# Performance work log

Measured on AMD Instinct MI355X. Metric: run time of the kernel, lower is better.

## Reference

```python
import jax, jax.numpy as jnp
import numpy as np

B, L, H, N, CH = 8, 2048, 512, 64, 1


def setup_inputs() -> dict:
    key = jax.random.key(0)
    ks = jax.random.split(key, 7)
    # S4D-Lin style init: w = -0.5 + i*pi*n, with slight noise on the real part
    w_re = -(0.5 + 0.1 * jax.random.uniform(ks[0], (H, N), dtype=jnp.float32))
    w_im = jnp.broadcast_to(jnp.pi * jnp.arange(N, dtype=jnp.float32), (H, N)).copy()
    C_re = jax.random.normal(ks[1], (CH, H, N), dtype=jnp.float32)
    C_im = jax.random.normal(ks[2], (CH, H, N), dtype=jnp.float32)
    D = jax.random.normal(ks[3], (CH, H), dtype=jnp.float32)
    # log-uniform dt in [1e-3, 1e-1]
    log_dt = jax.random.uniform(ks[4], (H,), dtype=jnp.float32,
                                minval=jnp.log(1e-3), maxval=jnp.log(1e-1))
    dt = jnp.exp(log_dt)
    u = jax.random.normal(ks[5], (B, L, H), dtype=jnp.float32)
    return {"u": u, "w_re": w_re, "w_im": w_im, "C_re": C_re,
            "C_im": C_im, "D": D, "dt": dt}


def reference(u, w_re, w_im, C_re, C_im, D, dt):
    # u: [B, L, H] -> [B, H, L]
    uT = jnp.swapaxes(u, -1, -2)
    l = uT.shape[-1]
    h = dt.shape[-1]
    w = (w_re + 1j * w_im).astype(jnp.complex64)          # [t, n]
    v = h // w.shape[0]
    w = jnp.tile(w, (v, 1))                                # [h, n]
    C = (C_re + 1j * C_im).astype(jnp.complex64)           # [c, h, n]
    # --- kernel generation ---
    dtA = w * dt[:, None]                                  # [h, n]
    K = jnp.arange(l) * dtA[..., None]                     # [h, n, l]
    Cs = C * ((jnp.exp(dtA) - 1.0) / w)                    # [c, h, n]
    k = 2.0 * jnp.einsum('chn,hnl->chl', Cs, jnp.exp(K)).real  # [c, h, l]
    # --- FFT convolution ---
    k_f = jnp.fft.rfft(k, n=2 * l - 1)                     # [c, h, l]
    u_f = jnp.fft.rfft(uT, n=2 * l - 1)                    # [B, h, l]
    y_f = jnp.einsum('...hl,chl->...chl', u_f, k_f)        # [B, c, h, l]
    y = jnp.fft.irfft(y_f, n=2 * l)[..., :l]               # [B, c, h, l]
    # skip connection
    y = y + jnp.einsum('...hl,ch->...chl', uT, D)
    # '... c h l -> ... l c h'
    return jnp.moveaxis(y, (-3, -2, -1), (-2, -1, -3))
```

## Files before the change

### kernel.cpp

```cpp
#include <hip/hip_runtime.h>
#include <hip/hip_bf16.h>
#include <math.h>


namespace {
constexpr int cB = 8;
constexpr int cL = 2048;
constexpr int cH = 512;
constexpr int cN = 64;
constexpr int M1 = 4095;
constexpr int M2 = 4096;
constexpr int BH = cB * cH;
constexpr int MA = BH + cH;

constexpr size_t S0   = 2 * ((size_t)cH * cN * 6);
constexpr size_t S_B1 = S0;
constexpr size_t S_A  = S_B1 + (size_t)4096 * 2048;
constexpr size_t S_T2 = S_A  + (size_t)MA * 2048;
constexpr size_t S_U  = S_T2 + (size_t)2048 * 4096;
}

typedef __attribute__((ext_vector_type(8))) short short8;
typedef __attribute__((ext_vector_type(4))) short sh4;
typedef __attribute__((ext_vector_type(4))) float f32x4;

static __device__ inline short f2bf(float x) {
    __hip_bfloat16 h = __float2bfloat16(x);
    return *reinterpret_cast<short*>(&h);
}
static __device__ inline float bf2f(short s) {
    return __uint_as_float(((unsigned int)(unsigned short)s) << 16);
}
static __device__ __forceinline__ void load_lds16(const short* g, short* l) {
    __builtin_amdgcn_global_load_lds(
        (const __attribute__((address_space(1))) void*)g,
        (__attribute__((address_space(3))) void*)l, 16, 0, 0);
}
#define WAIT_LGKM0() do { asm volatile("s_waitcnt lgkmcnt(0)" ::: "memory"); \
                          __builtin_amdgcn_sched_barrier(0); } while (0)
#define WAIT_VM(n)   do { asm volatile("s_waitcnt vmcnt(" #n ")" ::: "memory"); \
                          __builtin_amdgcn_sched_barrier(0); } while (0)

__global__ __launch_bounds__(256) void k_tabs(short* __restrict__ Wb)
{
    if (blockIdx.x < 2048) {
        int j  = blockIdx.x;
        int t0 = threadIdx.x * 8;
        int p  = (int)(((long)j * t0) % M1);
        short8 vc, vs;
#pragma unroll
        for (int i = 0; i < 8; ++i) {
            float s, c;
            sincosf((6.283185307179586f / (float)M1) * (float)p, &s, &c);
            vc[i] = f2bf(c); vs[i] = f2bf(s);
            p += j; if (p >= M1) p -= M1;
        }
        *(short8*)&Wb[S_B1 + (size_t)(2 * j)     * 2048 + t0] = vc;
        *(short8*)&Wb[S_B1 + (size_t)(2 * j + 1) * 2048 + t0] = vs;
    } else {
        int t  = blockIdx.x - 2048;
        int j0 = threadIdx.x * 8;
        int p  = (t * j0) & (M2 - 1);
        short8 vc, vs;
#pragma unroll
        for (int i = 0; i < 8; ++i) {
            float s, c;
            sincosf((6.283185307179586f / (float)M2) * (float)p, &s, &c);
            vc[i] = f2bf(c); vs[i] = f2bf(s);
            p = (p + t) & (M2 - 1);
        }
        *(short8*)&Wb[S_T2 + (size_t)t * 4096 + j0]        = vc;
        *(short8*)&Wb[S_T2 + (size_t)t * 4096 + 2048 + j0] = vs;
    }
}

__global__ __launch_bounds__(256) void k_trans(const float* __restrict__ u,
                                               short* __restrict__ Wb)
{
    __shared__ float tile[64][65];
    int t0 = blockIdx.x * 64;
    int h0 = blockIdx.y * 64;
    int b  = blockIdx.z;
    int cx = threadIdx.x & 63, r0 = threadIdx.x >> 6;
#pragma unroll
    for (int i = 0; i < 16; ++i) {
        int row = r0 + i * 4;
        tile[row][cx] = u[((size_t)b * cL + t0 + row) * cH + h0 + cx];
    }
    __syncthreads();
    short* A = Wb + S_A;
#pragma unroll
    for (int i = 0; i < 16; ++i) {
        int hrow = r0 + i * 4;
        A[(size_t)(b * cH + h0 + hrow) * 2048 + t0 + cx] = f2bf(tile[cx][hrow]);
    }
}

__global__ __launch_bounds__(256) void k_kgen(
    const float* __restrict__ w_re, const float* __restrict__ w_im,
    const float* __restrict__ C_re, const float* __restrict__ C_im,
    const float* __restrict__ dt, short* __restrict__ Wb)
{
    __shared__ float md[cN * 6];
    int h = blockIdx.x, tid = threadIdx.x;
    if (tid < cN) {
        int idx = h * cN + tid;
        double dtv = dt[h];
        double wr = w_re[idx], wi = w_im[idx];
        double ar = wr * dtv, ai = wi * dtv;
        double er = exp(ar);
        double zs, zc; sincos(ai, &zs, &zc);
        double zr = er * zc, zi = er * zs;
        double nr = zr - 1.0, ni = zi;
        double inv = 1.0 / (wr * wr + wi * wi);
        double gr = (nr * wr + ni * wi) * inv;
        double gi = (ni * wr - nr * wi) * inv;
        double cr = C_re[idx], ci = C_im[idx];
        md[tid*6+0] = (float)(cr * gr - ci * gi);
        md[tid*6+1] = (float)(cr * gi + ci * gr);
        md[tid*6+2] = (float)zr; md[tid*6+3] = (float)zi;
        md[tid*6+4] = (float)ar; md[tid*6+5] = (float)ai;
    }
    __syncthreads();
    int t0 = tid * 8;
    float acc[8] = {0.f, 0.f, 0.f, 0.f, 0.f, 0.f, 0.f, 0.f};
    for (int n = 0; n < cN; ++n) {
        float csr = md[n*6+0], csi = md[n*6+1];
        float zr  = md[n*6+2], zi  = md[n*6+3];
        float ar  = md[n*6+4], ai  = md[n*6+5];
        float mag = expf(ar * (float)t0);
        double ph = fmod((double)ai * (double)t0, 6.283185307179586);
        float s, c; sincosf((float)ph, &s, &c);
        float pr = mag * c, pi = mag * s;
#pragma unroll
        for (int i = 0; i < 8; ++i) {
            acc[i] += csr * pr - csi * pi;
            float tr = pr * zr - pi * zi;
            pi = pr * zi + pi * zr;
            pr = tr;
        }
    }
    short8 v;
#pragma unroll
    for (int i = 0; i < 8; ++i) v[i] = f2bf(2.f * acc[i]);
    *reinterpret_cast<short8*>(&Wb[S_A + (size_t)(BH + h) * 2048 + t0]) = v;
}

__device__ __forceinline__ void gemm8p_core(
    const short* __restrict__ Ag, int lda,
    const short* __restrict__ Bg, int ldb,
    int m0, int n0, int nt, short* lds, f32x4 (&acc)[4][4][2])
{
    const int tid  = threadIdx.x;
    const int wave = tid >> 6, lane = tid & 63;
    const int wm = wave >> 2, wn = wave & 3;
    const int lm = lane & 15, lk = lane >> 4;
    const int srow8 = lane >> 3;
    const int scol  = (lane & 7) * 8;

    auto stage = [&](const short* G, int ldg, int row0, int half, int kt, int sb) {
        short* l0 = lds + sb + (size_t)((kt & 1) * 2 + half) * 8192;
#pragma unroll
        for (int q = 0; q < 2; ++q) {
            int chunk = wave * 2 + q;
            int r = chunk * 8 + srow8;
            int c = scol ^ ((r & 7) << 3);
            load_lds16(G + (size_t)(row0 + half * 128 + r) * ldg + kt * 64 + c,
                       l0 + chunk * 512);
        }
    };
    auto rdA = [&](int qa, int kt, int mi, int kk) -> short8 {
        int rl = wm * 64 + mi * 16 + lm;
        int c  = (kk * 32 + lk * 8) ^ ((rl & 7) << 3);
        return *(const short8*)(lds + (size_t)((kt & 1) * 2 + qa) * 8192 + rl * 64 + c);
    };
    auto rdB = [&](int qb, int kt, int ni, int kk) -> short8 {
        int rl = wn * 32 + ni * 16 + lm;
        int c  = (kk * 32 + lk * 8) ^ ((rl & 7) << 3);
        return *(const short8*)(lds + 32768 + (size_t)((kt & 1) * 2 + qb) * 8192 + rl * 64 + c);
    };

    stage(Ag, lda, m0, 0, 0, 0);
    stage(Bg, ldb, n0, 0, 0, 32768);
    stage(Bg, ldb, n0, 1, 0, 32768);
    stage(Ag, lda, m0, 1, 0, 0);
    if (nt > 1) { stage(Ag, lda, m0, 0, 1, 0); stage(Bg, ldb, n0, 1, 1, 32768); }
    WAIT_VM(4);
    __builtin_amdgcn_s_barrier();

    short8 a[4][2], b[2][2];
    for (int t = 0; t < nt; ++t) {
#pragma unroll
        for (int mi = 0; mi < 4; ++mi) { a[mi][0] = rdA(0, t, mi, 0); a[mi][1] = rdA(0, t, mi, 1); }
#pragma unroll
        for (int ni = 0; ni < 2; ++ni) { b[ni][0] = rdB(0, t, ni, 0); b[ni][1] = rdB(0, t, ni, 1); }
        if (t + 1 < nt) stage(Ag, lda, m0, 1, t + 1, 0);
        __builtin_amdgcn_s_barrier();
        WAIT_LGKM0();
        __builtin_amdgcn_s_setprio(1);
#pragma unroll
        for (int kk = 0; kk < 2; ++kk)
#pragma unroll
        for (int ni = 0; ni < 2; ++ni)
#pragma unroll
        for (int mi = 0; mi < 4; ++mi)
            acc[0][mi][ni] = __builtin_amdgcn_mfma_f32_16x16x32_bf16(a[mi][kk], b[ni][kk], acc[0][mi][ni], 0, 0, 0);
        __builtin_amdgcn_s_setprio(0);
        __builtin_amdgcn_s_barrier();
#pragma unroll
        for (int ni = 0; ni < 2; ++ni) { b[ni][0] = rdB(1, t, ni, 0); b[ni][1] = rdB(1, t, ni, 1); }
        if (t + 1 < nt) stage(Bg, ldb, n0, 0, t + 1, 32768);
        __builtin_amdgcn_s_barrier();
        WAIT_LGKM0();
        __builtin_amdgcn_s_setprio(1);
#pragma unroll
        for (int kk = 0; kk < 2; ++kk)
#pragma unroll
        for (int ni = 0; ni < 2; ++ni)
#pragma unroll
        for (int mi = 0; mi < 4; ++mi)
            acc[1][mi][ni] = __builtin_amdgcn_mfma_f32_16x16x32_bf16(a[mi][kk], b[ni][kk], acc[1][mi][ni], 0, 0, 0);
        __builtin_amdgcn_s_setprio(0);
        __builtin_amdgcn_s_barrier();
#pragma unroll
        for (int mi = 0; mi < 4; ++mi) { a[mi][0] = rdA(1, t, mi, 0); a[mi][1] = rdA(1, t, mi, 1); }
        if (t + 2 < nt) stage(Ag, lda, m0, 0, t + 2, 0);
        __builtin_amdgcn_s_barrier();
        WAIT_LGKM0();
        __builtin_amdgcn_s_setprio(1);
#pragma unroll
        for (int kk = 0; kk < 2; ++kk)
#pragma unroll
        for (int ni = 0; ni < 2; ++ni)
#pragma unroll
        for (int mi = 0; mi < 4; ++mi)
            acc[3][mi][ni] = __builtin_amdgcn_mfma_f32_16x16x32_bf16(a[mi][kk], b[ni][kk], acc[3][mi][ni], 0, 0, 0);
        __builtin_amdgcn_s_setprio(0);
        __builtin_amdgcn_s_barrier();
#pragma unroll
        for (int ni = 0; ni < 2; ++ni) { b[ni][0] = rdB(0, t, ni, 0); b[ni][1] = rdB(0, t, ni, 1); }
        if (t + 2 < nt) stage(Bg, ldb, n0, 1, t + 2, 32768);
        if (t < nt - 2) { WAIT_VM(4); } else { WAIT_VM(0); }
        __builtin_amdgcn_s_barrier();
        WAIT_LGKM0();
        __builtin_amdgcn_s_setprio(1);
#pragma unroll
        for (int kk = 0; kk < 2; ++kk)
#pragma unroll
        for (int ni = 0; ni < 2; ++ni)
#pragma unroll
        for (int mi = 0; mi < 4; ++mi)
            acc[2][mi][ni] = __builtin_amdgcn_mfma_f32_16x16x32_bf16(a[mi][kk], b[ni][kk], acc[2][mi][ni], 0, 0, 0);
        __builtin_amdgcn_s_setprio(0);
        __builtin_amdgcn_s_barrier();
    }
}

__global__ __launch_bounds__(512, 2) void k_fwd8(short* __restrict__ Wb)
{
    __shared__ short lds_s[65536];
    int tile = (blockIdx.x & 7) * 32 + (blockIdx.x >> 3);
    const int m0 = (tile >> 4) * 256, n0 = (tile & 15) * 256;
    const int tid = threadIdx.x;
    const int wave = tid >> 6, lane = tid & 63;
    const int wm = wave >> 2, wn = wave & 3;
    const int lm = lane & 15, lk = lane >> 4;

    f32x4 acc[4][4][2] = {};
    gemm8p_core(Wb + S_A, 2048, Wb + S_B1, 2048, m0, n0, 32, lds_s, acc);

    short* Ys = Wb + S_U;
    const short* KF = Wb + S_U;
    short (*M)[136] = (short(*)[136])lds_s;
    for (int q = 0; q < 4; ++q) {
        __syncthreads();
#pragma unroll
        for (int mi = 0; mi < 4; ++mi)
#pragma unroll
        for (int ni = 0; ni < 2; ++ni)
#pragma unroll
        for (int r = 0; r < 4; ++r)
            M[wm * 64 + mi * 16 + lk * 4 + r][wn * 32 + ni * 16 + lm] =
                f2bf(acc[q][mi][ni][r]);
        __syncthreads();
        const int jwin = (n0 >> 1) + (q & 1) * 64;
#pragma unroll
        for (int pass = 0; pass < 4; ++pass) {
            int rl = pass * 32 + (tid >> 4);
            int p0 = (tid & 15) * 4;
            int rowg = m0 + (q >> 1) * 128 + rl;
            int h = rowg & (cH - 1);
            short8 kf8 = *(const short8*)&KF[(size_t)(4096 + h) * 4096 + 2 * (jwin + p0)];
            short8 m8  = *(const short8*)&M[rl][2 * p0];
            sh4 yr4, yi4;
#pragma unroll
            for (int i = 0; i < 4; ++i) {
                float C  = bf2f(m8[2*i]),  S  = bf2f(m8[2*i+1]);
                float Ck = bf2f(kf8[2*i]), Sk = bf2f(kf8[2*i+1]);
                int j = jwin + p0 + i;
                float sc = (j == 0 ? 1.0f : 2.0f) * (1.0f / (float)M2);
                yr4[i] = f2bf(sc * (Ck * C - Sk * S));
                yi4[i] = f2bf(sc * (Ck * S + Sk * C));
            }
            *(sh4*)&Ys[(size_t)rowg * 4096 + jwin + p0]        = yr4;
            *(sh4*)&Ys[(size_t)rowg * 4096 + 2048 + jwin + p0] = yi4;
        }
    }
}

__global__ __launch_bounds__(256, 2) void k_kfg(short* __restrict__ Wb)
{
    __shared__ __align__(16) short As[128][32];
    __shared__ __align__(16) short Bs[128][32];
    const short* A = Wb + S_A;
    const short* B = Wb + S_B1;
    short* U = Wb + S_U;
    const int tid = threadIdx.x;
    const int m0 = 4096 + blockIdx.y * 128, n0 = blockIdx.x * 128;
    const int wave = tid >> 6, lane = tid & 63;
    const int wr = wave >> 1, wc = wave & 1;
    const int lm = lane & 15, lk = lane >> 4;
    const int srow = lane >> 2, scol = (lane & 3) * 8;

    f32x4 acc[4][4] = {};
    for (int k0 = 0; k0 < 2048; k0 += 32) {
        __syncthreads();
        {
            int c0 = wave * 2;
            load_lds16(&A[(size_t)(m0 + c0*16      + srow)*2048 + k0 + scol], &As[c0*16][0]);
            load_lds16(&A[(size_t)(m0 + c0*16 + 16 + srow)*2048 + k0 + scol], &As[c0*16+16][0]);
            load_lds16(&B[(size_t)(n0 + c0*16      + srow)*2048 + k0 + scol], &Bs[c0*16][0]);
            load_lds16(&B[(size_t)(n0 + c0*16 + 16 + srow)*2048 + k0 + scol], &Bs[c0*16+16][0]);
        }
        __syncthreads();
        short8 a[4];
#pragma unroll
        for (int mi = 0; mi < 4; ++mi)
            a[mi] = *(const short8*)&As[wr*64 + mi*16 + lm][lk*8];
#pragma unroll
        for (int ni = 0; ni < 4; ++ni) {
            short8 b = *(const short8*)&Bs[wc*64 + ni*16 + lm][lk*8];
#pragma unroll
            for (int mi = 0; mi < 4; ++mi)
                acc[mi][ni] = __builtin_amdgcn_mfma_f32_16x16x32_bf16(a[mi], b, acc[mi][ni], 0, 0, 0);
        }
    }
#pragma unroll
    for (int mi = 0; mi < 4; ++mi)
#pragma unroll
    for (int ni = 0; ni < 4; ++ni)
#pragma unroll
    for (int r = 0; r < 4; ++r) {
        int row = m0 + wr*64 + mi*16 + lk*4 + r;
        int col = n0 + wc*64 + ni*16 + lm;
        U[(size_t)row * 4096 + col] = f2bf(acc[mi][ni][r]);
    }
}

__global__ __launch_bounds__(512, 1) void k_invB(const float* __restrict__ u,
                                                 const float* __restrict__ Dp,
                                                 short* __restrict__ Wb,
                                                 float* __restrict__ out)
{
    __shared__ short lds_s[49152];
    int tile = (blockIdx.x & 7) * 32 + (blockIdx.x >> 3);
    const int m0 = (tile >> 4) * 256;
    const int n0 = (tile & 15) * 128;
    const int tid = threadIdx.x;
    const int wave = tid >> 6, lane = tid & 63;
    const int wm = wave >> 2, wn = wave & 3;
    const int lm = lane & 15, lk = lane >> 4;
    const int srow8 = lane >> 3;
    const int scol  = (lane & 7) * 8;
    constexpr int nt = 64;
    short* lds = lds_s;
    const short* Ag = Wb + S_U;
    const short* Bg = Wb + S_T2;

    auto stageA = [&](int half, int kt) {
        short* l0 = lds + (size_t)((kt & 1) * 2 + half) * 8192;
#pragma unroll
        for (int q = 0; q < 2; ++q) {
            int chunk = wave * 2 + q;
            int r = chunk * 8 + srow8;
            int c = scol ^ ((r & 7) << 3);
            load_lds16(Ag + (size_t)(m0 + half * 128 + r) * 4096 + kt * 64 + c,
                       l0 + chunk * 512);
        }
    };
    auto stageB = [&](int kt) {
        short* l0 = lds + 32768 + (size_t)(kt & 1) * 8192;
#pragma unroll
        for (int q = 0; q < 2; ++q) {
            int chunk = wave * 2 + q;
            int r = chunk * 8 + srow8;
            int c = scol ^ ((r & 7) << 3);
            load_lds16(Bg + (size_t)(n0 + r) * 4096 + kt * 64 + c,
                       l0 + chunk * 512);
        }
    };
    auto rdA = [&](int half, int kt, int mi, int kk) -> short8 {
        int rl = wm * 64 + mi * 16 + lm;
        int c  = (kk * 32 + lk * 8) ^ ((rl & 7) << 3);
        return *(const short8*)(lds + (size_t)((kt & 1) * 2 + half) * 8192 + rl * 64 + c);
    };
    auto rdB = [&](int kt, int ni, int kk) -> short8 {
        int rl = wn * 32 + ni * 16 + lm;
        int c  = (kk * 32 + lk * 8) ^ ((rl & 7) << 3);
        return *(const short8*)(lds + 32768 + (size_t)(kt & 1) * 8192 + rl * 64 + c);
    };

    f32x4 acc[2][4][2] = {};

    stageA(0, 0);
    stageB(0);
    stageA(1, 0);
    WAIT_VM(2);
    __builtin_amdgcn_s_barrier();

    short8 a[4][2], b[2][2];
    for (int t = 0; t < nt; ++t) {
#pragma unroll
        for (int mi = 0; mi < 4; ++mi) { a[mi][0] = rdA(0, t, mi, 0); a[mi][1] = rdA(0, t, mi, 1); }
#pragma unroll
        for (int ni = 0; ni < 2; ++ni) { b[ni][0] = rdB(t, ni, 0); b[ni][1] = rdB(t, ni, 1); }
        if (t + 1 < nt) stageB(t + 1);
        __builtin_amdgcn_s_barrier();
        WAIT_LGKM0();
        __builtin_amdgcn_s_setprio(1);
#pragma unroll
        for (int kk = 0; kk < 2; ++kk)
#pragma unroll
        for (int ni = 0; ni < 2; ++ni)
#pragma unroll
        for (int mi = 0; mi < 4; ++mi)
            acc[0][mi][ni] = __builtin_amdgcn_mfma_f32_16x16x32_bf16(a[mi][kk], b[ni][kk], acc[0][mi][ni], 0, 0, 0);
        __builtin_amdgcn_s_setprio(0);
        if (t + 1 < nt) { WAIT_VM(2); } else { WAIT_VM(0); }
        __builtin_amdgcn_s_barrier();
#pragma unroll
        for (int mi = 0; mi < 4; ++mi) { a[mi][0] = rdA(1, t, mi, 0); a[mi][1] = rdA(1, t, mi, 1); }
        if (t + 1 < nt) { stageA(0, t + 1); stageA(1, t + 1); }
        __builtin_amdgcn_s_barrier();
        WAIT_LGKM0();
        __builtin_amdgcn_s_setprio(1);
#pragma unroll
        for (int kk = 0; kk < 2; ++kk)
#pragma unroll
        for (int ni = 0; ni < 2; ++ni)
#pragma unroll
        for (int mi = 0; mi < 4; ++mi)
            acc[1][mi][ni] = __builtin_amdgcn_mfma_f32_16x16x32_bf16(a[mi][kk], b[ni][kk], acc[1][mi][ni], 0, 0, 0);
        __builtin_amdgcn_s_setprio(0);
        WAIT_VM(2);
        __builtin_amdgcn_s_barrier();
    }

    const int b_  = m0 >> 9;
    const int h00 = m0 & 511;
    float (*T)[132] = (float(*)[132])lds_s;
#pragma unroll
    for (int q = 0; q < 2; ++q) {
        __syncthreads();
#pragma unroll
        for (int mi = 0; mi < 4; ++mi)
#pragma unroll
        for (int ni = 0; ni < 2; ++ni) {
            int tl = wn * 32 + ni * 16 + lm;
            int hl = wm * 64 + mi * 16 + lk * 4;
            *(float4*)&T[tl][hl] = *(float4*)&acc[q][mi][ni];
        }
        __syncthreads();
        int hg = h00 + q * 128 + (tid & 31) * 4;
        float4 dv = *(const float4*)&Dp[hg];
#pragma unroll
        for (int it = 0; it < 8; ++it) {
            int tl = (tid >> 5) + it * 16;
            int tg = n0 + tl;
            size_t gidx = ((size_t)b_ * cL + tg) * cH + hg;
            float4 uv = *(const float4*)&u[gidx];
            float4 yv = *(float4*)&T[tl][(tid & 31) * 4];
            yv.x += dv.x * uv.x;
            yv.y += dv.y * uv.y;
            yv.z += dv.z * uv.z;
            yv.w += dv.w * uv.w;
            *(float4*)&out[gidx] = yv;
        }
    }
}

extern "C" void kernel_launch(void* const* d_in, const int* in_sizes, int n_in,
                              void* d_out, int out_size, void* d_ws, size_t ws_size,
                              hipStream_t stream) {
    const float* u    = (const float*)d_in[0];
    const float* w_re = (const float*)d_in[1];
    const float* w_im = (const float*)d_in[2];
    const float* C_re = (const float*)d_in[3];
    const float* C_im = (const float*)d_in[4];
    const float* Dp   = (const float*)d_in[5];
    const float* dt   = (const float*)d_in[6];
    float* out = (float*)d_out;
    short* Wb  = (short*)d_ws;

    hipLaunchKernelGGL(k_tabs,  dim3(4096), dim3(256), 0, stream, Wb);
    hipLaunchKernelGGL(k_trans, dim3(cL / 64, cH / 64, cB), dim3(256), 0, stream, u, Wb);
    hipLaunchKernelGGL(k_kgen,  dim3(cH), dim3(256), 0, stream,
                       w_re, w_im, C_re, C_im, dt, Wb);
    hipLaunchKernelGGL(k_kfg,   dim3(32, 4), dim3(256), 0, stream, Wb);
    hipLaunchKernelGGL(k_fwd8,  dim3(256), dim3(512), 0, stream, Wb);
    hipLaunchKernelGGL(k_invB,  dim3(256), dim3(512), 0, stream, u, Dp, Wb, out);
}
```

Baseline: 228.4 us.

## Merge prep kernels and deepen GEMM prefetch pipelines with extra stage buffers

Merges the twiddle-table, transpose and kernel-generation launches into one k_prep kernel that dispatches on block index, removing two launches and their serialization. The gemm8p_core loop now prefetches two k-tiles ahead with separate A/B register sets, which reorders the quadrant MFMAs to reuse fragments. k_invB gets a third B stage buffer (LDS grows to 57344 shorts) so B can be prefetched three tiles ahead. In exchange, larger LDS and register use may lower occupancy, and the vmcnt wait counts must match the new issue order exactly.

```diff
diff --git a/kernel.cpp b/kernel.cpp
--- a/kernel.cpp
+++ b/kernel.cpp
@@ -40,12 +40,19 @@
                           __builtin_amdgcn_sched_barrier(0); } while (0)
 #define WAIT_VM(n)   do { asm volatile("s_waitcnt vmcnt(" #n ")" ::: "memory"); \
                           __builtin_amdgcn_sched_barrier(0); } while (0)
-
-__global__ __launch_bounds__(256) void k_tabs(short* __restrict__ Wb)
+#define BAR() __builtin_amdgcn_s_barrier()
+
+__global__ __launch_bounds__(256) void k_prep(
+    const float* __restrict__ u,
+    const float* __restrict__ w_re, const float* __restrict__ w_im,
+    const float* __restrict__ C_re, const float* __restrict__ C_im,
+    const float* __restrict__ dt, short* __restrict__ Wb)
 {
-    if (blockIdx.x < 2048) {
-        int j  = blockIdx.x;
-        int t0 = threadIdx.x * 8;
+    __shared__ char smc[64 * 65 * 4];
+    int bid = blockIdx.x, tid = threadIdx.x;
+    if (bid < 2048) {
+        int j  = bid;
+        int t0 = tid * 8;
         int p  = (int)(((long)j * t0) % M1);
         short8 vc, vs;
 #pragma unroll
@@ -57,9 +64,9 @@
         }
         *(short8*)&Wb[S_B1 + (size_t)(2 * j)     * 2048 + t0] = vc;
         *(short8*)&Wb[S_B1 + (size_t)(2 * j + 1) * 2048 + t0] = vs;
-    } else {
-        int t  = blockIdx.x - 2048;
-        int j0 = threadIdx.x * 8;
+    } else if (bid < 4096) {
+        int t  = bid - 2048;
+        int j0 = tid * 8;
         int p  = (t * j0) & (M2 - 1);
         short8 vc, vs;
 #pragma unroll
@@ -71,80 +78,77 @@
         }
         *(short8*)&Wb[S_T2 + (size_t)t * 4096 + j0]        = vc;
         *(short8*)&Wb[S_T2 + (size_t)t * 4096 + 2048 + j0] = vs;
-    }
-}
-
-__global__ __launch_bounds__(256) void k_trans(const float* __restrict__ u,
-                                               short* __restrict__ Wb)
-{
-    __shared__ float tile[64][65];
-    int t0 = blockIdx.x * 64;
-    int h0 = blockIdx.y * 64;
-    int b  = blockIdx.z;
-    int cx = threadIdx.x & 63, r0 = threadIdx.x >> 6;
-#pragma unroll
-    for (int i = 0; i < 16; ++i) {
-        int row = r0 + i * 4;
-        tile[row][cx] = u[((size_t)b * cL + t0 + row) * cH + h0 + cx];
-    }
-    __syncthreads();
-    short* A = Wb + S_A;
-#pragma unroll
-    for (int i = 0; i < 16; ++i) {
-        int hrow = r0 + i * 4;
-        A[(size_t)(b * cH + h0 + hrow) * 2048 + t0 + cx] = f2bf(tile[cx][hrow]);
-    }
-}
-
-__global__ __launch_bounds__(256) void k_kgen(
-    const float* __restrict__ w_re, const float* __restrict__ w_im,
-    const float* __restrict__ C_re, const float* __restrict__ C_im,
-    const float* __restrict__ dt, short* __restrict__ Wb)
-{
-    __shared__ float md[cN * 6];
-    int h = blockIdx.x, tid = threadIdx.x;
-    if (tid < cN) {
-        int idx = h * cN + tid;
-        double dtv = dt[h];
-        double wr = w_re[idx], wi = w_im[idx];
-        double ar = wr * dtv, ai = wi * dtv;
-        double er = exp(ar);
-        double zs, zc; sincos(ai, &zs, &zc);
-        double zr = er * zc, zi = er * zs;
-        double nr = zr - 1.0, ni = zi;
-        double inv = 1.0 / (wr * wr + wi * wi);
-        double gr = (nr * wr + ni * wi) * inv;
-        double gi = (ni * wr - nr * wi) * inv;
-        double cr = C_re[idx], ci = C_im[idx];
-        md[tid*6+0] = (float)(cr * gr - ci * gi);
-        md[tid*6+1] = (float)(cr * gi + ci * gr);
-        md[tid*6+2] = (float)zr; md[tid*6+3] = (float)zi;
-        md[tid*6+4] = (float)ar; md[tid*6+5] = (float)ai;
-    }
-    __syncthreads();
-    int t0 = tid * 8;
-    float acc[8] = {0.f, 0.f, 0.f, 0.f, 0.f, 0.f, 0.f, 0.f};
-    for (int n = 0; n < cN; ++n) {
-        float csr = md[n*6+0], csi = md[n*6+1];
-        float zr  = md[n*6+2], zi  = md[n*6+3];
-        float ar  = md[n*6+4], ai  = md[n*6+5];
-        float mag = expf(ar * (float)t0);
-        double ph = fmod((double)ai * (double)t0, 6.283185307179586);
-        float s, c; sincosf((float)ph, &s, &c);
-        float pr = mag * c, pi = mag * s;
-#pragma unroll
-        for (int i = 0; i < 8; ++i) {
-            acc[i] += csr * pr - csi * pi;
-            float tr = pr * zr - pi * zi;
-            pi = pr * zi + pi * zr;
-            pr = tr;
-        }
-    }
-    short8 v;
-#pragma unroll
-    for (int i = 0; i < 8; ++i) v[i] = f2bf(2.f * acc[i]);
-    *reinterpret_cast<short8*>(&Wb[S_A + (size_t)(BH + h) * 2048 + t0]) = v;
-}
+    } else if (bid < 6144) {
+        float (*tile)[65] = (float(*)[65])smc;
+        int bid2 = bid - 4096;
+        int t0 = (bid2 & 31) * 64;
+        int h0 = ((bid2 >> 5) & 7) * 64;
+        int b  = bid2 >> 8;
+        int cx = tid & 63, r0 = tid >> 6;
+#pragma unroll
+        for (int i = 0; i < 16; ++i) {
+            int row = r0 + i * 4;
+            tile[row][cx] = u[((size_t)b * cL + t0 + row) * cH + h0 + cx];
+        }
+        __syncthreads();
+        short* A = Wb + S_A;
+#pragma unroll
+        for (int i = 0; i < 16; ++i) {
+            int hrow = r0 + i * 4;
+            A[(size_t)(b * cH + h0 + hrow) * 2048 + t0 + cx] = f2bf(tile[cx][hrow]);
+        }
+    } else {
+        float* md = (float*)smc;
+        int h = bid - 6144;
+        if (tid < cN) {
+            int idx = h * cN + tid;
+            double dtv = dt[h];
+            double wr = w_re[idx], wi = w_im[idx];
+            double ar = wr * dtv, ai = wi * dtv;
+            double er = exp(ar);
+            double zs, zc; sincos(ai, &zs, &zc);
+            double zr = er * zc, zi = er * zs;
+            double nr = zr - 1.0, ni = zi;
+            double inv = 1.0 / (wr * wr + wi * wi);
+            double gr = (nr * wr + ni * wi) * inv;
+            double gi = (ni * wr - nr * wi) * inv;
+            double cr = C_re[idx], ci = C_im[idx];
+            md[tid*6+0] = (float)(cr * gr - ci * gi);
+            md[tid*6+1] = (float)(cr * gi + ci * gr);
+            md[tid*6+2] = (float)zr; md[tid*6+3] = (float)zi;
+            md[tid*6+4] = (float)ar; md[tid*6+5] = (float)ai;
+        }
+        __syncthreads();
+        int t0 = tid * 8;
+        float acc[8] = {0.f, 0.f, 0.f, 0.f, 0.f, 0.f, 0.f, 0.f};
+        for (int n = 0; n < cN; ++n) {
+            float csr = md[n*6+0], csi = md[n*6+1];
+            float zr  = md[n*6+2], zi  = md[n*6+3];
+            float ar  = md[n*6+4], ai  = md[n*6+5];
+            float mag = expf(ar * (float)t0);
+            double ph = fmod((double)ai * (double)t0, 6.283185307179586);
+            float s, c; sincosf((float)ph, &s, &c);
+            float pr = mag * c, pi = mag * s;
+#pragma unroll
+            for (int i = 0; i < 8; ++i) {
+                acc[i] += csr * pr - csi * pi;
+                float tr = pr * zr - pi * zi;
+                pi = pr * zi + pi * zr;
+                pr = tr;
+            }
+        }
+        short8 v;
+#pragma unroll
+        for (int i = 0; i < 8; ++i) v[i] = f2bf(2.f * acc[i]);
+        *reinterpret_cast<short8*>(&Wb[S_A + (size_t)(BH + h) * 2048 + t0]) = v;
+    }
+}
+
+#define MFMA16(AR, BR, ACC) \
+    _Pragma("unroll") for (int kk = 0; kk < 2; ++kk) \
+    _Pragma("unroll") for (int ni = 0; ni < 2; ++ni) \
+    _Pragma("unroll") for (int mi = 0; mi < 4; ++mi) \
+        ACC[mi][ni] = __builtin_amdgcn_mfma_f32_16x16x32_bf16(AR[mi][kk], BR[ni][kk], ACC[mi][ni], 0, 0, 0);
 
 __device__ __forceinline__ void gemm8p_core(
     const short* __restrict__ Ag, int lda,
@@ -184,75 +188,52 @@
     stage(Bg, ldb, n0, 0, 0, 32768);
     stage(Bg, ldb, n0, 1, 0, 32768);
     stage(Ag, lda, m0, 1, 0, 0);
-    if (nt > 1) { stage(Ag, lda, m0, 0, 1, 0); stage(Bg, ldb, n0, 1, 1, 32768); }
-    WAIT_VM(4);
-    __builtin_amdgcn_s_barrier();
-
-    short8 a[4][2], b[2][2];
+    stage(Ag, lda, m0, 0, 1, 0);
+    stage(Bg, ldb, n0, 0, 1, 32768);
+    stage(Bg, ldb, n0, 1, 1, 32768);
+    stage(Ag, lda, m0, 1, 1, 0);
+    WAIT_VM(12);
+    BAR();
+
+    short8 a0[4][2], a1[4][2], b0[2][2], b1[2][2];
     for (int t = 0; t < nt; ++t) {
-#pragma unroll
-        for (int mi = 0; mi < 4; ++mi) { a[mi][0] = rdA(0, t, mi, 0); a[mi][1] = rdA(0, t, mi, 1); }
-#pragma unroll
-        for (int ni = 0; ni < 2; ++ni) { b[ni][0] = rdB(0, t, ni, 0); b[ni][1] = rdB(0, t, ni, 1); }
-        if (t + 1 < nt) stage(Ag, lda, m0, 1, t + 1, 0);
-        __builtin_amdgcn_s_barrier();
+        const bool st = (t + 2 < nt);
+#pragma unroll
+        for (int mi = 0; mi < 4; ++mi) { a0[mi][0] = rdA(0, t, mi, 0); a0[mi][1] = rdA(0, t, mi, 1); }
+#pragma unroll
+        for (int ni = 0; ni < 2; ++ni) { b0[ni][0] = rdB(0, t, ni, 0); b0[ni][1] = rdB(0, t, ni, 1); }
+        BAR();
         WAIT_LGKM0();
         __builtin_amdgcn_s_setprio(1);
-#pragma unroll
-        for (int kk = 0; kk < 2; ++kk)
-#pragma unroll
-        for (int ni = 0; ni < 2; ++ni)
-#pragma unroll
-        for (int mi = 0; mi < 4; ++mi)
-            acc[0][mi][ni] = __builtin_amdgcn_mfma_f32_16x16x32_bf16(a[mi][kk], b[ni][kk], acc[0][mi][ni], 0, 0, 0);
-        __builtin_amdgcn_s_setprio(0);
-        __builtin_amdgcn_s_barrier();
-#pragma unroll
-        for (int ni = 0; ni < 2; ++ni) { b[ni][0] = rdB(1, t, ni, 0); b[ni][1] = rdB(1, t, ni, 1); }
-        if (t + 1 < nt) stage(Bg, ldb, n0, 0, t + 1, 32768);
-        __builtin_amdgcn_s_barrier();
+        MFMA16(a0, b0, acc[0]);
+        __builtin_amdgcn_s_setprio(0);
+        if (st) { WAIT_VM(10); } else { WAIT_VM(0); }
+        BAR();
+#pragma unroll
+        for (int ni = 0; ni < 2; ++ni) { b1[ni][0] = rdB(1, t, ni, 0); b1[ni][1] = rdB(1, t, ni, 1); }
+        if (st) { stage(Ag, lda, m0, 0, t + 2, 0); stage(Bg, ldb, n0, 0, t + 2, 32768); }
+        BAR();
         WAIT_LGKM0();
         __builtin_amdgcn_s_setprio(1);
-#pragma unroll
-        for (int kk = 0; kk < 2; ++kk)
-#pragma unroll
-        for (int ni = 0; ni < 2; ++ni)
-#pragma unroll
-        for (int mi = 0; mi < 4; ++mi)
-            acc[1][mi][ni] = __builtin_amdgcn_mfma_f32_16x16x32_bf16(a[mi][kk], b[ni][kk], acc[1][mi][ni], 0, 0, 0);
-        __builtin_amdgcn_s_setprio(0);
-        __builtin_amdgcn_s_barrier();
-#pragma unroll
-        for (int mi = 0; mi < 4; ++mi) { a[mi][0] = rdA(1, t, mi, 0); a[mi][1] = rdA(1, t, mi, 1); }
-        if (t + 2 < nt) stage(Ag, lda, m0, 0, t + 2, 0);
-        __builtin_amdgcn_s_barrier();
+        MFMA16(a0, b1, acc[1]);
+        __builtin_amdgcn_s_setprio(0);
+        if (st) { WAIT_VM(12); } else { WAIT_VM(0); }
+        BAR();
+#pragma unroll
+        for (int mi = 0; mi < 4; ++mi) { a1[mi][0] = rdA(1, t, mi, 0); a1[mi][1] = rdA(1, t, mi, 1); }
+        if (st) stage(Bg, ldb, n0, 1, t + 2, 32768);
+        BAR();
         WAIT_LGKM0();
         __builtin_amdgcn_s_setprio(1);
-#pragma unroll
-        for (int kk = 0; kk < 2; ++kk)
-#pragma unroll
-        for (int ni = 0; ni < 2; ++ni)
-#pragma unroll
-        for (int mi = 0; mi < 4; ++mi)
-            acc[3][mi][ni] = __builtin_amdgcn_mfma_f32_16x16x32_bf16(a[mi][kk], b[ni][kk], acc[3][mi][ni], 0, 0, 0);
-        __builtin_amdgcn_s_setprio(0);
-        __builtin_amdgcn_s_barrier();
-#pragma unroll
-        for (int ni = 0; ni < 2; ++ni) { b[ni][0] = rdB(0, t, ni, 0); b[ni][1] = rdB(0, t, ni, 1); }
-        if (t + 2 < nt) stage(Bg, ldb, n0, 1, t + 2, 32768);
-        if (t < nt - 2) { WAIT_VM(4); } else { WAIT_VM(0); }
-        __builtin_amdgcn_s_barrier();
-        WAIT_LGKM0();
-        __builtin_amdgcn_s_setprio(1);
-#pragma unroll
-        for (int kk = 0; kk < 2; ++kk)
-#pragma unroll
-        for (int ni = 0; ni < 2; ++ni)
-#pragma unroll
-        for (int mi = 0; mi < 4; ++mi)
-            acc[2][mi][ni] = __builtin_amdgcn_mfma_f32_16x16x32_bf16(a[mi][kk], b[ni][kk], acc[2][mi][ni], 0, 0, 0);
-        __builtin_amdgcn_s_setprio(0);
-        __builtin_amdgcn_s_barrier();
+        MFMA16(a1, b1, acc[3]);
+        __builtin_amdgcn_s_setprio(0);
+        BAR();
+        if (st) stage(Ag, lda, m0, 1, t + 2, 0);
+        __builtin_amdgcn_s_setprio(1);
+        MFMA16(a1, b0, acc[2]);
+        __builtin_amdgcn_s_setprio(0);
+        if (st) { WAIT_VM(12); } else { WAIT_VM(0); }
+        BAR();
     }
 }
 
@@ -362,7 +343,7 @@
                                                  short* __restrict__ Wb,
                                                  float* __restrict__ out)
 {
-    __shared__ short lds_s[49152];
+    __shared__ short lds_s[57344];
     int tile = (blockIdx.x & 7) * 32 + (blockIdx.x >> 3);
     const int m0 = (tile >> 4) * 256;
     const int n0 = (tile & 15) * 128;
@@ -388,8 +369,8 @@
                        l0 + chunk * 512);
         }
     };
-    auto stageB = [&](int kt) {
-        short* l0 = lds + 32768 + (size_t)(kt & 1) * 8192;
+    auto stageB = [&](int kt, int slot) {
+        short* l0 = lds + 32768 + (size_t)slot * 8192;
 #pragma unroll
         for (int q = 0; q < 2; ++q) {
             int chunk = wave * 2 + q;
@@ -404,56 +385,51 @@
         int c  = (kk * 32 + lk * 8) ^ ((rl & 7) << 3);
         return *(const short8*)(lds + (size_t)((kt & 1) * 2 + half) * 8192 + rl * 64 + c);
     };
-    auto rdB = [&](int kt, int ni, int kk) -> short8 {
+    auto rdB = [&](int slot, int ni, int kk) -> short8 {
         int rl = wn * 32 + ni * 16 + lm;
         int c  = (kk * 32 + lk * 8) ^ ((rl & 7) << 3);
-        return *(const short8*)(lds + 32768 + (size_t)(kt & 1) * 8192 + rl * 64 + c);
+        return *(const short8*)(lds + 32768 + (size_t)slot * 8192 + rl * 64 + c);
     };
 
     f32x4 acc[2][4][2] = {};
 
     stageA(0, 0);
-    stageB(0);
+    stageB(0, 0);
     stageA(1, 0);
-    WAIT_VM(2);
-    __builtin_amdgcn_s_barrier();
+    stageA(0, 1);
+    stageB(1, 1);
+    stageB(2, 2);
+    WAIT_VM(6);
+    BAR();
 
     short8 a[4][2], b[2][2];
+    int bs = 0;
     for (int t = 0; t < nt; ++t) {
+        const bool deep = (t + 3 < nt);
 #pragma unroll
         for (int mi = 0; mi < 4; ++mi) { a[mi][0] = rdA(0, t, mi, 0); a[mi][1] = rdA(0, t, mi, 1); }
 #pragma unroll
-        for (int ni = 0; ni < 2; ++ni) { b[ni][0] = rdB(t, ni, 0); b[ni][1] = rdB(t, ni, 1); }
-        if (t + 1 < nt) stageB(t + 1);
-        __builtin_amdgcn_s_barrier();
+        for (int ni = 0; ni < 2; ++ni) { b[ni][0] = rdB(bs, ni, 0); b[ni][1] = rdB(bs, ni, 1); }
+        if (t + 1 < nt) stageA(1, t + 1);
+        BAR();
         WAIT_LGKM0();
         __builtin_amdgcn_s_setprio(1);
-#pragma unroll
-        for (int kk = 0; kk < 2; ++kk)
-#pragma unroll
-        for (int ni = 0; ni < 2; ++ni)
-#pragma unroll
-        for (int mi = 0; mi < 4; ++mi)
-            acc[0][mi][ni] = __builtin_amdgcn_mfma_f32_16x16x32_bf16(a[mi][kk], b[ni][kk], acc[0][mi][ni], 0, 0, 0);
-        __builtin_amdgcn_s_setprio(0);
-        if (t + 1 < nt) { WAIT_VM(2); } else { WAIT_VM(0); }
-        __builtin_amdgcn_s_barrier();
+        MFMA16(a, b, acc[0]);
+        __builtin_amdgcn_s_setprio(0);
+        if (deep) { WAIT_VM(6); } else { WAIT_VM(0); }
+        BAR();
 #pragma unroll
         for (int mi = 0; mi < 4; ++mi) { a[mi][0] = rdA(1, t, mi, 0); a[mi][1] = rdA(1, t, mi, 1); }
-        if (t + 1 < nt) { stageA(0, t + 1); stageA(1, t + 1); }
-        __builtin_amdgcn_s_barrier();
+        if (t + 2 < nt) stageA(0, t + 2);
+        if (t + 3 < nt) stageB(t + 3, bs);
+        BAR();
         WAIT_LGKM0();
         __builtin_amdgcn_s_setprio(1);
-#pragma unroll
-        for (int kk = 0; kk < 2; ++kk)
-#pragma unroll
-        for (int ni = 0; ni < 2; ++ni)
-#pragma unroll
-        for (int mi = 0; mi < 4; ++mi)
-            acc[1][mi][ni] = __builtin_amdgcn_mfma_f32_16x16x32_bf16(a[mi][kk], b[ni][kk], acc[1][mi][ni], 0, 0, 0);
-        __builtin_amdgcn_s_setprio(0);
-        WAIT_VM(2);
-        __builtin_amdgcn_s_barrier();
+        MFMA16(a, b, acc[1]);
+        __builtin_amdgcn_s_setprio(0);
+        if (deep) { WAIT_VM(6); } else { WAIT_VM(0); }
+        BAR();
+        bs = (bs == 2) ? 0 : bs + 1;
     }
 
     const int b_  = m0 >> 9;
@@ -502,10 +478,8 @@
     float* out = (float*)d_out;
     short* Wb  = (short*)d_ws;
 
-    hipLaunchKernelGGL(k_tabs,  dim3(4096), dim3(256), 0, stream, Wb);
-    hipLaunchKernelGGL(k_trans, dim3(cL / 64, cH / 64, cB), dim3(256), 0, stream, u, Wb);
-    hipLaunchKernelGGL(k_kgen,  dim3(cH), dim3(256), 0, stream,
-                       w_re, w_im, C_re, C_im, dt, Wb);
+    hipLaunchKernelGGL(k_prep,  dim3(6656), dim3(256), 0, stream,
+                       u, w_re, w_im, C_re, C_im, dt, Wb);
     hipLaunchKernelGGL(k_kfg,   dim3(32, 4), dim3(256), 0, stream, Wb);
     hipLaunchKernelGGL(k_fwd8,  dim3(256), dim3(512), 0, stream, Wb);
     hipLaunchKernelGGL(k_invB,  dim3(256), dim3(512), 0, stream, u, Dp, Wb, out);
```

New measurement: 255.6 us. 1.12x slower.
